# Kernel tuning notes

Hardware: AMD Instinct MI355X
Metric: run time of the kernel (lower is better)

The kernel has to match this reference:

```python
import jax, jax.numpy as jnp
import numpy as np

E = 1024
H = E // 2


def setup_inputs() -> dict:
    key = jax.random.key(0)
    ks = jax.random.split(key, 12)
    s = 0.02
    inp = {
        'long_x': jax.random.normal(ks[0], (4096, 64, E), jnp.float32),
        'encoded_x': jax.random.normal(ks[1], (512, 64, E), jnp.float32),
        'sp_w1': jax.random.normal(ks[2], (E, H), jnp.float32) * s,
        'sp_b1': jnp.zeros((H,), jnp.float32),
        'sp_w2': jax.random.normal(ks[3], (H, 2), jnp.float32) * s,
        'sp_b2': jnp.zeros((2,), jnp.float32),
        'rs_w1': jax.random.normal(ks[4], (2 * E, H), jnp.float32) * s,
        'rs_b1': jnp.zeros((H,), jnp.float32),
        'rs_w2': jax.random.normal(ks[5], (H, 1), jnp.float32) * s,
        'rs_b2': jnp.zeros((1,), jnp.float32),
        'fu_w': jax.random.normal(ks[6], (2 * E, E), jnp.float32) * s,
        'fu_b': jnp.zeros((E,), jnp.float32),
        'g_w': jax.random.normal(ks[7], (E, E), jnp.float32) * s,
        'g_b': jnp.zeros((E,), jnp.float32),
        'decay_l': jnp.asarray(0.9, jnp.float32),
        'decay_g': jnp.asarray(0.8, jnp.float32),
    }
    return inp


def _gelu(x):
    return jax.nn.gelu(x, approximate=False)


def _pooled(hist, ctx, decay, rs_w1, rs_b1, rs_w2, rs_b2):
    # hist: [L, B, E]; ctx: [B, E]
    L = hist.shape[0]
    comb = jnp.concatenate([hist, jnp.broadcast_to(ctx[None], hist.shape)], axis=-1)  # [L,B,2E]
    scores = jax.nn.sigmoid(_gelu(comb @ rs_w1 + rs_b1) @ rs_w2 + rs_b2)[..., 0]  # [L,B]
    pos = jnp.arange(L, dtype=hist.dtype)
    dec = decay ** (L - 1 - pos)  # [L]
    w = jax.nn.softmax(scores + jnp.log(dec + 1e-8)[:, None], axis=0)  # [L,B]
    return jnp.einsum('lb,lbe->be', w, hist)


def reference(long_x, encoded_x, sp_w1, sp_b1, sp_w2, sp_b2,
              rs_w1, rs_b1, rs_w2, rs_b2, fu_w, fu_b, g_w, g_b,
              decay_l, decay_g):
    seq_len, batch, _ = long_x.shape
    ctx = jnp.mean(encoded_x, axis=0)  # [B,E]
    span_w = jax.nn.softmax(_gelu(ctx @ sp_w1 + sp_b1) @ sp_w2 + sp_b2, axis=-1)  # [B,2]

    local_span = min(8 * 4, seq_len)  # min_span*4
    local_hist = long_x[seq_len - local_span:]  # [local_span,B,E]
    local_feat = _pooled(local_hist, ctx, decay_l, rs_w1, rs_b1, rs_w2, rs_b2)

    step = max(1, seq_len // 32) if seq_len > 32 else 1
    global_hist = long_x[::step] if seq_len > 32 else long_x
    global_feat = _pooled(global_hist, ctx, decay_g, rs_w1, rs_b1, rs_w2, rs_b2)

    combined = jnp.concatenate([local_feat * span_w[:, 0:1], global_feat * span_w[:, 1:2]], axis=-1)
    fused = _gelu(combined @ fu_w + fu_b)  # [B,E]
    gate = jax.nn.sigmoid(fused @ g_w + g_b)
    adaptive = fused * gate

    attn = jnp.full((seq_len, batch), 1.0 / seq_len, dtype=long_x.dtype)
    return attn, adaptive
```

## Files before the change

### kernel.cpp

```cpp
#include <hip/hip_runtime.h>

typedef __attribute__((ext_vector_type(8))) short bf16x8;
typedef __attribute__((ext_vector_type(4))) float f32x4;

#define WS_CTXPROJ  0
#define WS_SPANPART 32768
#define WS_PART     33792
#define WS_FEATS    66560
#define WS_FUSED    197632
#define WS_PBUF     263168
#define WS_PBUFA    787456
#define WS_PBUFB    1836032
#define WS_APACK    2884608
#define WS_BPACK    7078912

__device__ __forceinline__ float gelu_f(float x) {
    return 0.5f * x * (1.0f + erff(x * 0.70710678118654752f));
}
__device__ __forceinline__ float sigm_f(float x) {
    return 1.0f / (1.0f + expf(-x));
}
__device__ __forceinline__ short f2bf(float f) {
    unsigned u = __float_as_uint(f);
    u += 0x7fffu + ((u >> 16) & 1u);
    return (short)(u >> 16);
}
__device__ __forceinline__ void f2bf2(float f, short& hi, short& lo) {
    hi = f2bf(f);
    float fh = __uint_as_float(((unsigned)(unsigned short)hi) << 16);
    lo = f2bf(f - fh);
}

__device__ __forceinline__ int row_to_s(int r) {
    int p = r >> 11, pos = (r & 2047) >> 6;
    return p ? pos * 128 : 4064 + pos;
}

__global__ __launch_bounds__(256) void prep_k(const float* __restrict__ long_x,
                                              const float* __restrict__ enc,
                                              const float* __restrict__ rs_w1,
                                              float* __restrict__ pbuf,
                                              short* __restrict__ Apack,
                                              short* __restrict__ Bpack,
                                              float* __restrict__ attn_out) {
    int blk = blockIdx.x, t = threadIdx.x;
    if (blk < 512) {
        int gt = blk * 256 + t;
        int chunk = gt >> 14, idx = gt & 16383;
        const float4* src = reinterpret_cast<const float4*>(enc) + idx;
        float sx = 0.f, sy = 0.f, sz = 0.f, sw = 0.f;
        int s0 = chunk * 64;
        for (int s = s0; s < s0 + 64; ++s) {
            float4 v = src[(size_t)s * 16384];
            sx += v.x; sy += v.y; sz += v.z; sw += v.w;
        }
        float4 o; o.x = sx; o.y = sy; o.z = sz; o.w = sw;
        reinterpret_cast<float4*>(pbuf)[(size_t)chunk * 16384 + idx] = o;
    } else if (blk < 1024) {
        int ti = (blk - 512) * 256 + t;
        int r  = ti >> 5, kt = ti & 31;
        int b  = r & 63;
        int s  = row_to_s(r);
        const float4* src = reinterpret_cast<const float4*>(
            long_x + ((size_t)s * 64 + b) * 1024 + kt * 32);
        float fs[32];
        #pragma unroll
        for (int q = 0; q < 8; ++q) {
            float4 v = src[q];
            fs[q * 4 + 0] = v.x; fs[q * 4 + 1] = v.y;
            fs[q * 4 + 2] = v.z; fs[q * 4 + 3] = v.w;
        }
        int mt = r >> 4, lo16 = r & 15;
        bf16x8* dst = reinterpret_cast<bf16x8*>(Apack);
        #pragma unroll
        for (int hi4 = 0; hi4 < 4; ++hi4) {
            bf16x8 h, l;
            #pragma unroll
            for (int j = 0; j < 8; ++j) {
                short hi, lo; f2bf2(fs[hi4 * 8 + j], hi, lo);
                h[j] = hi; l[j] = lo;
            }
            size_t idx = ((size_t)(mt * 32 + kt) * 64 + hi4 * 16 + lo16) * 2;
            dst[idx]     = h;
            dst[idx + 1] = l;
        }
    } else if (blk < 1280) {
        int ti = (blk - 1024) * 256 + t;
        int lane = ti & 63, kt = (ti >> 6) & 31, nt = ti >> 11;
        int k0 = kt * 32 + (lane >> 4) * 8;
        int col = nt * 16 + (lane & 15);
        bf16x8 h, l;
        #pragma unroll
        for (int j = 0; j < 8; ++j) {
            short hi, lo; f2bf2(rs_w1[(size_t)(k0 + j) * 512 + col], hi, lo);
            h[j] = hi; l[j] = lo;
        }
        reinterpret_cast<bf16x8*>(Bpack)[ti * 2]     = h;
        reinterpret_cast<bf16x8*>(Bpack)[ti * 2 + 1] = l;
    } else {
        int i = (blk - 1280) * 256 + t;
        float4 v; v.x = v.y = v.z = v.w = (1.0f / 4096.0f);
        reinterpret_cast<float4*>(attn_out)[i] = v;
    }
}

__global__ __launch_bounds__(256) void heads_k(const float* __restrict__ pbuf,
                                               const float* __restrict__ rs_w1,
                                               const float* __restrict__ rs_b1,
                                               const float* __restrict__ sp_w1,
                                               const float* __restrict__ sp_b1,
                                               const float* __restrict__ sp_w2,
                                               const float* __restrict__ sp_b2,
                                               float* __restrict__ ctxproj,
                                               float* __restrict__ spanpart) {
    __shared__ float c4[4][1024];
    __shared__ float sums[4][64][4];
    __shared__ float r0[4][64], r1[4][64];
    int blk = blockIdx.x, t = threadIdx.x;
    int role = blk >> 7;
    int bq = (blk >> 3) & 15, jc = blk & 7;
    int b0 = bq * 4, j0 = jc * 64;
    for (int e = t; e < 4096; e += 256) {
        int b = e >> 10, k = e & 1023;
        float s = 0.f;
        #pragma unroll
        for (int cc = 0; cc < 8; ++cc) s += pbuf[((size_t)(cc * 64 + b0 + b)) * 1024 + k];
        c4[b][k] = s * (1.0f / 512.0f);
    }
    __syncthreads();
    int jl = t & 63, kh = t >> 6;
    int j = j0 + jl;
    const float* w = (role == 0 ? rs_w1 + (size_t)1024 * 512 : sp_w1)
                     + (size_t)(kh * 256) * 512 + j;
    float acc[4] = {0.f, 0.f, 0.f, 0.f};
    #pragma unroll 8
    for (int k = 0; k < 256; ++k) {
        float wv = w[(size_t)k * 512];
        int kk = kh * 256 + k;
        acc[0] += c4[0][kk] * wv;
        acc[1] += c4[1][kk] * wv;
        acc[2] += c4[2][kk] * wv;
        acc[3] += c4[3][kk] * wv;
    }
    #pragma unroll
    for (int b = 0; b < 4; ++b) sums[kh][jl][b] = acc[b];
    __syncthreads();
    {
        int jl2 = t >> 2, b = t & 3;
        float val = sums[0][jl2][b] + sums[1][jl2][b] + sums[2][jl2][b] + sums[3][jl2][b];
        int jj = j0 + jl2, gb = b0 + b;
        if (role == 0) {
            ctxproj[(size_t)gb * 512 + jj] = rs_b1[jj] + val;
        } else {
            float h = gelu_f(sp_b1[jj] + val);
            r0[b][jl2] = h * sp_w2[jj * 2 + 0];
            r1[b][jl2] = h * sp_w2[jj * 2 + 1];
        }
    }
    if (role == 1) {
        __syncthreads();
        for (int s = 32; s > 0; s >>= 1) {
            if (t < 4 * s) {
                int bb = t / s, qq = t % s;
                r0[bb][qq] += r0[bb][qq + s];
                r1[bb][qq] += r1[bb][qq + s];
            }
            __syncthreads();
        }
        if (t < 4) {
            spanpart[((size_t)(b0 + t) * 8 + jc) * 2 + 0] = r0[t][0];
            spanpart[((size_t)(b0 + t) * 8 + jc) * 2 + 1] = r1[t][0];
        }
    }
}

__global__ __launch_bounds__(256) void score_mfma_k(const short* __restrict__ Apack_,
                                                    const short* __restrict__ Bpack_,
                                                    const float* __restrict__ ctxproj,
                                                    const float* __restrict__ rs_w2,
                                                    float* __restrict__ part) {
    const bf16x8* Apack = reinterpret_cast<const bf16x8*>(Apack_);
    const bf16x8* Bpack = reinterpret_cast<const bf16x8*>(Bpack_);
    int t = threadIdx.x, lane = t & 63, w = t >> 6;
    int wr = w & 1, wc = w >> 1;
    int bm = blockIdx.x & 63, bn = blockIdx.x >> 6;
    int mt0 = bm * 4 + wr * 2;
    int nt0 = bn * 8 + wc * 4;
    f32x4 acc[2][4];
    #pragma unroll
    for (int r = 0; r < 2; ++r)
        #pragma unroll
        for (int i = 0; i < 4; ++i) acc[r][i] = (f32x4){0.f, 0.f, 0.f, 0.f};
    const bf16x8* A0 = Apack + ((size_t)(mt0 + 0) * 32 * 64 + lane) * 2;
    const bf16x8* A1 = Apack + ((size_t)(mt0 + 1) * 32 * 64 + lane) * 2;
    const bf16x8* B0 = Bpack + ((size_t)(nt0 + 0) * 32 * 64 + lane) * 2;
    const bf16x8* B1 = Bpack + ((size_t)(nt0 + 1) * 32 * 64 + lane) * 2;
    const bf16x8* B2 = Bpack + ((size_t)(nt0 + 2) * 32 * 64 + lane) * 2;
    const bf16x8* B3 = Bpack + ((size_t)(nt0 + 3) * 32 * 64 + lane) * 2;
    #pragma unroll 2
    for (int kt = 0; kt < 32; ++kt) {
        bf16x8 a0h = A0[kt * 128], a0l = A0[kt * 128 + 1];
        bf16x8 a1h = A1[kt * 128], a1l = A1[kt * 128 + 1];
        bf16x8 bh[4], bl[4];
        bh[0] = B0[kt * 128]; bl[0] = B0[kt * 128 + 1];
        bh[1] = B1[kt * 128]; bl[1] = B1[kt * 128 + 1];
        bh[2] = B2[kt * 128]; bl[2] = B2[kt * 128 + 1];
        bh[3] = B3[kt * 128]; bl[3] = B3[kt * 128 + 1];
        #pragma unroll
        for (int i = 0; i < 4; ++i) {
            acc[0][i] = __builtin_amdgcn_mfma_f32_16x16x32_bf16(a0h, bh[i], acc[0][i], 0, 0, 0);
            acc[1][i] = __builtin_amdgcn_mfma_f32_16x16x32_bf16(a1h, bh[i], acc[1][i], 0, 0, 0);
        }
        #pragma unroll
        for (int i = 0; i < 4; ++i) {
            acc[0][i] = __builtin_amdgcn_mfma_f32_16x16x32_bf16(a0h, bl[i], acc[0][i], 0, 0, 0);
            acc[1][i] = __builtin_amdgcn_mfma_f32_16x16x32_bf16(a1h, bl[i], acc[1][i], 0, 0, 0);
        }
        #pragma unroll
        for (int i = 0; i < 4; ++i) {
            acc[0][i] = __builtin_amdgcn_mfma_f32_16x16x32_bf16(a0l, bh[i], acc[0][i], 0, 0, 0);
            acc[1][i] = __builtin_amdgcn_mfma_f32_16x16x32_bf16(a1l, bh[i], acc[1][i], 0, 0, 0);
        }
    }
    int hi = lane >> 4, lo = lane & 15;
    int cc[4]; float w2[4];
    #pragma unroll
    for (int i = 0; i < 4; ++i) { cc[i] = (nt0 + i) * 16 + lo; w2[i] = rs_w2[cc[i]]; }
    float pl[8];
    #pragma unroll
    for (int rr = 0; rr < 2; ++rr) {
        #pragma unroll
        for (int reg = 0; reg < 4; ++reg) {
            int row = (mt0 + rr) * 16 + hi * 4 + reg;
            int b = row & 63;
            float s = 0.f;
            #pragma unroll
            for (int i = 0; i < 4; ++i)
                s += gelu_f(acc[rr][i][reg] + ctxproj[(size_t)b * 512 + cc[i]]) * w2[i];
            pl[rr * 4 + reg] = s;
        }
    }
    #pragma unroll
    for (int m = 1; m < 16; m <<= 1) {
        #pragma unroll
        for (int q = 0; q < 8; ++q) pl[q] += __shfl_xor(pl[q], m, 64);
    }
    if (lo == 0) {
        int chunk = bn * 2 + wc;
        #pragma unroll
        for (int rr = 0; rr < 2; ++rr)
            #pragma unroll
            for (int reg = 0; reg < 4; ++reg) {
                int row = (mt0 + rr) * 16 + hi * 4 + reg;
                part[(size_t)row * 8 + chunk] = pl[rr * 4 + reg];
            }
    }
}

__global__ __launch_bounds__(256) void pool_k(const float* __restrict__ long_x,
                                              const float* __restrict__ part,
                                              const float* __restrict__ rs_b2,
                                              const float* __restrict__ decay_l,
                                              const float* __restrict__ decay_g,
                                              float* __restrict__ feats) {
    __shared__ float red[32][8];
    __shared__ float wl[32];
    int blk = blockIdx.x;
    int p = blk >> 6, b = blk & 63;
    int t = threadIdx.x;
    {
        int pos = t >> 3, ccq = t & 7;
        red[pos][ccq] = part[(size_t)(p * 2048 + pos * 64 + b) * 8 + ccq];
    }
    __syncthreads();
    if (t < 32) {
        float z = rs_b2[0];
        #pragma unroll
        for (int q = 0; q < 8; ++q) z += red[t][q];
        float sc = sigm_f(z);
        float decay = p ? decay_g[0] : decay_l[0];
        float dec = powf(decay, (float)(31 - t));
        wl[t] = sc + logf(dec + 1e-8f);
    }
    __syncthreads();
    if (t == 0) {
        float m = -1e30f;
        for (int j = 0; j < 32; ++j) m = fmaxf(m, wl[j]);
        float ssum = 0.f;
        float e[32];
        for (int j = 0; j < 32; ++j) { e[j] = expf(wl[j] - m); ssum += e[j]; }
        float inv = 1.0f / ssum;
        for (int j = 0; j < 32; ++j) wl[j] = e[j] * inv;
    }
    __syncthreads();
    float sx = 0.f, sy = 0.f, sz = 0.f, sw = 0.f;
    #pragma unroll 8
    for (int l = 0; l < 32; ++l) {
        int s = p ? (l * 128) : (4064 + l);
        float4 v = reinterpret_cast<const float4*>(long_x)[((size_t)s * 64 + b) * 256 + t];
        float wv = wl[l];
        sx += wv * v.x; sy += wv * v.y; sz += wv * v.z; sw += wv * v.w;
    }
    float4 o; o.x = sx; o.y = sy; o.z = sz; o.w = sw;
    reinterpret_cast<float4*>(feats)[((size_t)(p * 64 + b)) * 256 + t] = o;
}

__global__ __launch_bounds__(256) void fu_partial_k(const float* __restrict__ feats,
                                                    const float* __restrict__ spanpart,
                                                    const float* __restrict__ sp_b2,
                                                    const float* __restrict__ fu_w,
                                                    float* __restrict__ pbufA) {
    __shared__ float a[64][132];
    __shared__ float sw[64][2];
    int kchunk = blockIdx.x >> 4;
    int nt     = blockIdx.x & 15;
    int t = threadIdx.x;
    if (t < 64) {
        float s0 = 0.f, s1 = 0.f;
        #pragma unroll
        for (int q = 0; q < 8; ++q) {
            s0 += spanpart[((size_t)t * 8 + q) * 2 + 0];
            s1 += spanpart[((size_t)t * 8 + q) * 2 + 1];
        }
        float l0 = s0 + sp_b2[0], l1 = s1 + sp_b2[1];
        float m = fmaxf(l0, l1);
        float e0 = expf(l0 - m), e1 = expf(l1 - m), inv = 1.0f / (e0 + e1);
        sw[t][0] = e0 * inv; sw[t][1] = e1 * inv;
    }
    __syncthreads();
    int p = kchunk >> 3, kbase = (kchunk & 7) * 128;
    int colq = t & 15, bg = t >> 4;
    #pragma unroll
    for (int it = 0; it < 8; ++it) {
        int idx = t + it * 256;
        int b = idx >> 5, kq = idx & 31;
        float4 v = *reinterpret_cast<const float4*>(
            feats + ((size_t)(p * 64 + b)) * 1024 + kbase + kq * 4);
        float sc = sw[b][p];
        v.x *= sc; v.y *= sc; v.z *= sc; v.w *= sc;
        *reinterpret_cast<float4*>(&a[b][kq * 4]) = v;
    }
    __syncthreads();
    float acc[4][4] = {};
    #pragma unroll 4
    for (int k = 0; k < 128; ++k) {
        float4 wv = *reinterpret_cast<const float4*>(
            fu_w + (size_t)(kchunk * 128 + k) * 1024 + nt * 64 + colq * 4);
        #pragma unroll
        for (int i = 0; i < 4; ++i) {
            float av = a[bg * 4 + i][k];
            acc[i][0] += av * wv.x; acc[i][1] += av * wv.y;
            acc[i][2] += av * wv.z; acc[i][3] += av * wv.w;
        }
    }
    #pragma unroll
    for (int i = 0; i < 4; ++i) {
        float4 o; o.x = acc[i][0]; o.y = acc[i][1]; o.z = acc[i][2]; o.w = acc[i][3];
        *reinterpret_cast<float4*>(
            pbufA + ((size_t)(kchunk * 64 + bg * 4 + i)) * 1024 + nt * 64 + colq * 4) = o;
    }
}

__global__ __launch_bounds__(256) void fu_final_k(const float* __restrict__ pbufA,
                                                  const float* __restrict__ fu_b,
                                                  float* __restrict__ fused) {
    int i4 = blockIdx.x * 256 + threadIdx.x;
    int bi = (i4 * 4) & 1023;
    float4 z; z.x = fu_b[bi]; z.y = fu_b[bi + 1]; z.z = fu_b[bi + 2]; z.w = fu_b[bi + 3];
    #pragma unroll
    for (int c = 0; c < 16; ++c) {
        float4 v = reinterpret_cast<const float4*>(pbufA)[(size_t)c * 16384 + i4];
        z.x += v.x; z.y += v.y; z.z += v.z; z.w += v.w;
    }
    float4 o;
    o.x = gelu_f(z.x); o.y = gelu_f(z.y); o.z = gelu_f(z.z); o.w = gelu_f(z.w);
    reinterpret_cast<float4*>(fused)[i4] = o;
}

__global__ __launch_bounds__(256) void g_partial_k(const float* __restrict__ fused,
                                                   const float* __restrict__ g_w,
                                                   float* __restrict__ pbufB) {
    __shared__ float a[64][68];
    int kchunk = blockIdx.x >> 4;
    int nt     = blockIdx.x & 15;
    int t = threadIdx.x;
    int k0 = kchunk * 64;
    #pragma unroll
    for (int it = 0; it < 4; ++it) {
        int idx = t + it * 256;
        int b = idx >> 4, kq = idx & 15;
        float4 z = *reinterpret_cast<const float4*>(fused + (size_t)b * 1024 + k0 + kq * 4);
        *reinterpret_cast<float4*>(&a[b][kq * 4]) = z;
    }
    __syncthreads();
    int colq = t & 15, bg = t >> 4;
    float acc[4][4] = {};
    #pragma unroll 4
    for (int k = 0; k < 64; ++k) {
        float4 wv = *reinterpret_cast<const float4*>(
            g_w + (size_t)(k0 + k) * 1024 + nt * 64 + colq * 4);
        #pragma unroll
        for (int i = 0; i < 4; ++i) {
            float av = a[bg * 4 + i][k];
            acc[i][0] += av * wv.x; acc[i][1] += av * wv.y;
            acc[i][2] += av * wv.z; acc[i][3] += av * wv.w;
        }
    }
    #pragma unroll
    for (int i = 0; i < 4; ++i) {
        float4 o; o.x = acc[i][0]; o.y = acc[i][1]; o.z = acc[i][2]; o.w = acc[i][3];
        *reinterpret_cast<float4*>(
            pbufB + ((size_t)(kchunk * 64 + bg * 4 + i)) * 1024 + nt * 64 + colq * 4) = o;
    }
}

__global__ __launch_bounds__(256) void g_final_k(const float* __restrict__ pbufB,
                                                 const float* __restrict__ g_b,
                                                 const float* __restrict__ fused,
                                                 float* __restrict__ out_adaptive) {
    int i4 = blockIdx.x * 256 + threadIdx.x;
    int bi = (i4 * 4) & 1023;
    float4 z; z.x = g_b[bi]; z.y = g_b[bi + 1]; z.z = g_b[bi + 2]; z.w = g_b[bi + 3];
    #pragma unroll
    for (int c = 0; c < 16; ++c) {
        float4 v = reinterpret_cast<const float4*>(pbufB)[(size_t)c * 16384 + i4];
        z.x += v.x; z.y += v.y; z.z += v.z; z.w += v.w;
    }
    float4 f = reinterpret_cast<const float4*>(fused)[i4];
    float4 o;
    o.x = f.x * sigm_f(z.x); o.y = f.y * sigm_f(z.y);
    o.z = f.z * sigm_f(z.z); o.w = f.w * sigm_f(z.w);
    reinterpret_cast<float4*>(out_adaptive)[i4] = o;
}

extern "C" void kernel_launch(void* const* d_in, const int* in_sizes, int n_in,
                              void* d_out, int out_size, void* d_ws, size_t ws_size,
                              hipStream_t stream) {
    const float* long_x  = (const float*)d_in[0];
    const float* enc     = (const float*)d_in[1];
    const float* sp_w1   = (const float*)d_in[2];
    const float* sp_b1   = (const float*)d_in[3];
    const float* sp_w2   = (const float*)d_in[4];
    const float* sp_b2   = (const float*)d_in[5];
    const float* rs_w1   = (const float*)d_in[6];
    const float* rs_b1   = (const float*)d_in[7];
    const float* rs_w2   = (const float*)d_in[8];
    const float* rs_b2   = (const float*)d_in[9];
    const float* fu_w    = (const float*)d_in[10];
    const float* fu_b    = (const float*)d_in[11];
    const float* g_w     = (const float*)d_in[12];
    const float* g_b     = (const float*)d_in[13];
    const float* decay_l = (const float*)d_in[14];
    const float* decay_g = (const float*)d_in[15];

    float* out = (float*)d_out;
    float* ws  = (float*)d_ws;

    prep_k<<<1536, 256, 0, stream>>>(long_x, enc, rs_w1, ws + WS_PBUF,
                                     (short*)(ws + WS_APACK), (short*)(ws + WS_BPACK), out);
    heads_k<<<256, 256, 0, stream>>>(ws + WS_PBUF, rs_w1, rs_b1, sp_w1, sp_b1, sp_w2, sp_b2,
                                     ws + WS_CTXPROJ, ws + WS_SPANPART);
    score_mfma_k<<<256, 256, 0, stream>>>((short*)(ws + WS_APACK), (short*)(ws + WS_BPACK),
                                          ws + WS_CTXPROJ, rs_w2, ws + WS_PART);
    pool_k<<<128, 256, 0, stream>>>(long_x, ws + WS_PART, rs_b2, decay_l, decay_g,
                                    ws + WS_FEATS);
    fu_partial_k<<<256, 256, 0, stream>>>(ws + WS_FEATS, ws + WS_SPANPART, sp_b2, fu_w,
                                          ws + WS_PBUFA);
    fu_final_k<<<64, 256, 0, stream>>>(ws + WS_PBUFA, fu_b, ws + WS_FUSED);
    g_partial_k<<<256, 256, 0, stream>>>(ws + WS_FUSED, g_w, ws + WS_PBUFB);
    g_final_k<<<64, 256, 0, stream>>>(ws + WS_PBUFB, g_b, ws + WS_FUSED, out + 262144);
}
```

Measured before the change: 118.7 us.

## Drop split-bf16 compensation in score GEMM and widen block to 512 threads

Replaces the hi/lo split-bf16 representation (three MFMAs per product to emulate fp32) with a single plain bf16 conversion of long_x and rs_w1. This halves the packed operand traffic and cuts the score GEMM's MFMA count by three. The score kernel now runs 8 waves per block, each handling 2 N-tiles instead of 4. Partial sums are written as 16 chunks rather than 8, and pool_k is updated to match. Score accuracy drops to plain bf16, which may cost precision in the attention softmax.

```diff
diff --git a/kernel.cpp b/kernel.cpp
--- a/kernel.cpp
+++ b/kernel.cpp
@@ -6,13 +6,13 @@
 #define WS_CTXPROJ  0
 #define WS_SPANPART 32768
 #define WS_PART     33792
-#define WS_FEATS    66560
-#define WS_FUSED    197632
-#define WS_PBUF     263168
-#define WS_PBUFA    787456
-#define WS_PBUFB    1836032
-#define WS_APACK    2884608
-#define WS_BPACK    7078912
+#define WS_FEATS    99328
+#define WS_FUSED    230400
+#define WS_PBUF     295936
+#define WS_PBUFA    820224
+#define WS_PBUFB    1868800
+#define WS_APACK    2917376
+#define WS_BPACK    5014528
 
 __device__ __forceinline__ float gelu_f(float x) {
     return 0.5f * x * (1.0f + erff(x * 0.70710678118654752f));
@@ -24,11 +24,6 @@
     unsigned u = __float_as_uint(f);
     u += 0x7fffu + ((u >> 16) & 1u);
     return (short)(u >> 16);
-}
-__device__ __forceinline__ void f2bf2(float f, short& hi, short& lo) {
-    hi = f2bf(f);
-    float fh = __uint_as_float(((unsigned)(unsigned short)hi) << 16);
-    lo = f2bf(f - fh);
 }
 
 __device__ __forceinline__ int row_to_s(int r) {
@@ -74,29 +69,20 @@
         bf16x8* dst = reinterpret_cast<bf16x8*>(Apack);
         #pragma unroll
         for (int hi4 = 0; hi4 < 4; ++hi4) {
-            bf16x8 h, l;
+            bf16x8 h;
             #pragma unroll
-            for (int j = 0; j < 8; ++j) {
-                short hi, lo; f2bf2(fs[hi4 * 8 + j], hi, lo);
-                h[j] = hi; l[j] = lo;
-            }
-            size_t idx = ((size_t)(mt * 32 + kt) * 64 + hi4 * 16 + lo16) * 2;
-            dst[idx]     = h;
-            dst[idx + 1] = l;
+            for (int j = 0; j < 8; ++j) h[j] = f2bf(fs[hi4 * 8 + j]);
+            dst[(size_t)(mt * 32 + kt) * 64 + hi4 * 16 + lo16] = h;
         }
     } else if (blk < 1280) {
         int ti = (blk - 1024) * 256 + t;
         int lane = ti & 63, kt = (ti >> 6) & 31, nt = ti >> 11;
         int k0 = kt * 32 + (lane >> 4) * 8;
         int col = nt * 16 + (lane & 15);
-        bf16x8 h, l;
-        #pragma unroll
-        for (int j = 0; j < 8; ++j) {
-            short hi, lo; f2bf2(rs_w1[(size_t)(k0 + j) * 512 + col], hi, lo);
-            h[j] = hi; l[j] = lo;
-        }
-        reinterpret_cast<bf16x8*>(Bpack)[ti * 2]     = h;
-        reinterpret_cast<bf16x8*>(Bpack)[ti * 2 + 1] = l;
+        bf16x8 h;
+        #pragma unroll
+        for (int j = 0; j < 8; ++j) h[j] = f2bf(rs_w1[(size_t)(k0 + j) * 512 + col]);
+        reinterpret_cast<bf16x8*>(Bpack)[ti] = h;
     } else {
         int i = (blk - 1280) * 256 + t;
         float4 v; v.x = v.y = v.z = v.w = (1.0f / 4096.0f);
@@ -174,7 +160,7 @@
     }
 }
 
-__global__ __launch_bounds__(256) void score_mfma_k(const short* __restrict__ Apack_,
+__global__ __launch_bounds__(512) void score_mfma_k(const short* __restrict__ Apack_,
                                                     const short* __restrict__ Bpack_,
                                                     const float* __restrict__ ctxproj,
                                                     const float* __restrict__ rs_w2,
@@ -185,47 +171,30 @@
     int wr = w & 1, wc = w >> 1;
     int bm = blockIdx.x & 63, bn = blockIdx.x >> 6;
     int mt0 = bm * 4 + wr * 2;
-    int nt0 = bn * 8 + wc * 4;
-    f32x4 acc[2][4];
+    int nt0 = bn * 8 + wc * 2;
+    f32x4 acc[2][2];
     #pragma unroll
     for (int r = 0; r < 2; ++r)
         #pragma unroll
-        for (int i = 0; i < 4; ++i) acc[r][i] = (f32x4){0.f, 0.f, 0.f, 0.f};
-    const bf16x8* A0 = Apack + ((size_t)(mt0 + 0) * 32 * 64 + lane) * 2;
-    const bf16x8* A1 = Apack + ((size_t)(mt0 + 1) * 32 * 64 + lane) * 2;
-    const bf16x8* B0 = Bpack + ((size_t)(nt0 + 0) * 32 * 64 + lane) * 2;
-    const bf16x8* B1 = Bpack + ((size_t)(nt0 + 1) * 32 * 64 + lane) * 2;
-    const bf16x8* B2 = Bpack + ((size_t)(nt0 + 2) * 32 * 64 + lane) * 2;
-    const bf16x8* B3 = Bpack + ((size_t)(nt0 + 3) * 32 * 64 + lane) * 2;
-    #pragma unroll 2
+        for (int i = 0; i < 2; ++i) acc[r][i] = (f32x4){0.f, 0.f, 0.f, 0.f};
+    const bf16x8* A0 = Apack + ((size_t)(mt0 + 0) * 2048 + lane);
+    const bf16x8* A1 = Apack + ((size_t)(mt0 + 1) * 2048 + lane);
+    const bf16x8* B0 = Bpack + ((size_t)(nt0 + 0) * 2048 + lane);
+    const bf16x8* B1 = Bpack + ((size_t)(nt0 + 1) * 2048 + lane);
+    #pragma unroll 4
     for (int kt = 0; kt < 32; ++kt) {
-        bf16x8 a0h = A0[kt * 128], a0l = A0[kt * 128 + 1];
-        bf16x8 a1h = A1[kt * 128], a1l = A1[kt * 128 + 1];
-        bf16x8 bh[4], bl[4];
-        bh[0] = B0[kt * 128]; bl[0] = B0[kt * 128 + 1];
-        bh[1] = B1[kt * 128]; bl[1] = B1[kt * 128 + 1];
-        bh[2] = B2[kt * 128]; bl[2] = B2[kt * 128 + 1];
-        bh[3] = B3[kt * 128]; bl[3] = B3[kt * 128 + 1];
-        #pragma unroll
-        for (int i = 0; i < 4; ++i) {
-            acc[0][i] = __builtin_amdgcn_mfma_f32_16x16x32_bf16(a0h, bh[i], acc[0][i], 0, 0, 0);
-            acc[1][i] = __builtin_amdgcn_mfma_f32_16x16x32_bf16(a1h, bh[i], acc[1][i], 0, 0, 0);
-        }
-        #pragma unroll
-        for (int i = 0; i < 4; ++i) {
-            acc[0][i] = __builtin_amdgcn_mfma_f32_16x16x32_bf16(a0h, bl[i], acc[0][i], 0, 0, 0);
-            acc[1][i] = __builtin_amdgcn_mfma_f32_16x16x32_bf16(a1h, bl[i], acc[1][i], 0, 0, 0);
-        }
-        #pragma unroll
-        for (int i = 0; i < 4; ++i) {
-            acc[0][i] = __builtin_amdgcn_mfma_f32_16x16x32_bf16(a0l, bh[i], acc[0][i], 0, 0, 0);
-            acc[1][i] = __builtin_amdgcn_mfma_f32_16x16x32_bf16(a1l, bh[i], acc[1][i], 0, 0, 0);
-        }
+        bf16x8 a0 = A0[kt * 64];
+        bf16x8 a1 = A1[kt * 64];
+        bf16x8 b0 = B0[kt * 64];
+        bf16x8 b1 = B1[kt * 64];
+        acc[0][0] = __builtin_amdgcn_mfma_f32_16x16x32_bf16(a0, b0, acc[0][0], 0, 0, 0);
+        acc[0][1] = __builtin_amdgcn_mfma_f32_16x16x32_bf16(a0, b1, acc[0][1], 0, 0, 0);
+        acc[1][0] = __builtin_amdgcn_mfma_f32_16x16x32_bf16(a1, b0, acc[1][0], 0, 0, 0);
+        acc[1][1] = __builtin_amdgcn_mfma_f32_16x16x32_bf16(a1, b1, acc[1][1], 0, 0, 0);
     }
     int hi = lane >> 4, lo = lane & 15;
-    int cc[4]; float w2[4];
-    #pragma unroll
-    for (int i = 0; i < 4; ++i) { cc[i] = (nt0 + i) * 16 + lo; w2[i] = rs_w2[cc[i]]; }
+    int c0 = (nt0 + 0) * 16 + lo, c1 = (nt0 + 1) * 16 + lo;
+    float w2c0 = rs_w2[c0], w2c1 = rs_w2[c1];
     float pl[8];
     #pragma unroll
     for (int rr = 0; rr < 2; ++rr) {
@@ -233,11 +202,9 @@
         for (int reg = 0; reg < 4; ++reg) {
             int row = (mt0 + rr) * 16 + hi * 4 + reg;
             int b = row & 63;
-            float s = 0.f;
-            #pragma unroll
-            for (int i = 0; i < 4; ++i)
-                s += gelu_f(acc[rr][i][reg] + ctxproj[(size_t)b * 512 + cc[i]]) * w2[i];
-            pl[rr * 4 + reg] = s;
+            pl[rr * 4 + reg] =
+                gelu_f(acc[rr][0][reg] + ctxproj[(size_t)b * 512 + c0]) * w2c0 +
+                gelu_f(acc[rr][1][reg] + ctxproj[(size_t)b * 512 + c1]) * w2c1;
         }
     }
     #pragma unroll
@@ -246,13 +213,13 @@
         for (int q = 0; q < 8; ++q) pl[q] += __shfl_xor(pl[q], m, 64);
     }
     if (lo == 0) {
-        int chunk = bn * 2 + wc;
+        int chunk = bn * 4 + wc;
         #pragma unroll
         for (int rr = 0; rr < 2; ++rr)
             #pragma unroll
             for (int reg = 0; reg < 4; ++reg) {
                 int row = (mt0 + rr) * 16 + hi * 4 + reg;
-                part[(size_t)row * 8 + chunk] = pl[rr * 4 + reg];
+                part[(size_t)row * 16 + chunk] = pl[rr * 4 + reg];
             }
     }
 }
@@ -263,20 +230,20 @@
                                               const float* __restrict__ decay_l,
                                               const float* __restrict__ decay_g,
                                               float* __restrict__ feats) {
-    __shared__ float red[32][8];
+    __shared__ float red[32][16];
     __shared__ float wl[32];
     int blk = blockIdx.x;
     int p = blk >> 6, b = blk & 63;
     int t = threadIdx.x;
-    {
-        int pos = t >> 3, ccq = t & 7;
-        red[pos][ccq] = part[(size_t)(p * 2048 + pos * 64 + b) * 8 + ccq];
+    for (int i = t; i < 512; i += 256) {
+        int pos = i >> 4, cc = i & 15;
+        red[pos][cc] = part[(size_t)(p * 2048 + pos * 64 + b) * 16 + cc];
     }
     __syncthreads();
     if (t < 32) {
         float z = rs_b2[0];
         #pragma unroll
-        for (int q = 0; q < 8; ++q) z += red[t][q];
+        for (int q = 0; q < 16; ++q) z += red[t][q];
         float sc = sigm_f(z);
         float decay = p ? decay_g[0] : decay_l[0];
         float dec = powf(decay, (float)(31 - t));
@@ -460,7 +427,7 @@
                                      (short*)(ws + WS_APACK), (short*)(ws + WS_BPACK), out);
     heads_k<<<256, 256, 0, stream>>>(ws + WS_PBUF, rs_w1, rs_b1, sp_w1, sp_b1, sp_w2, sp_b2,
                                      ws + WS_CTXPROJ, ws + WS_SPANPART);
-    score_mfma_k<<<256, 256, 0, stream>>>((short*)(ws + WS_APACK), (short*)(ws + WS_BPACK),
+    score_mfma_k<<<256, 512, 0, stream>>>((short*)(ws + WS_APACK), (short*)(ws + WS_BPACK),
                                           ws + WS_CTXPROJ, rs_w2, ws + WS_PART);
     pool_k<<<128, 256, 0, stream>>>(long_x, ws + WS_PART, rs_b2, decay_l, decay_g,
                                     ws + WS_FEATS);
```

Measured after the change: 105.4 us. -11.2%, faster.
